# Performance work log

Measured on AMD Instinct MI355X. Metric: run time of the kernel, lower is better.

## Reference

```python
import jax, jax.numpy as jnp
import numpy as np

CHANNELS = 32


def _mlp(x, W1, b1, W2, b2, W3, b3):
    # FNN: Linear -> ReLU -> Linear -> ReLU -> Linear (last layer linear)
    h = jax.nn.relu(x @ W1 + b1)
    h = jax.nn.relu(h @ W2 + b2)
    return h @ W3 + b3


def setup_inputs() -> dict:
    key = jax.random.key(0)
    ks = jax.random.split(key, 8)
    E = 262144
    C = CHANNELS
    H = 128
    d_in = 4  # 2 * spatial_dim
    d_out = C * (C + 1)  # 1056
    s = lambda fan_in: 1.0 / np.sqrt(fan_in)
    return {
        "pos_i": jax.random.normal(ks[0], (E, 2), jnp.float32),
        "pos_j": jax.random.normal(ks[1], (E, 2), jnp.float32),
        "v_j": jax.random.normal(ks[2], (E, C), jnp.float32),
        "W1": jax.random.normal(ks[3], (d_in, H), jnp.float32) * s(d_in),
        "b1": jnp.zeros((H,), jnp.float32),
        "W2": jax.random.normal(ks[4], (H, H), jnp.float32) * s(H),
        "b2": jnp.zeros((H,), jnp.float32),
        "W3": jax.random.normal(ks[5], (H, d_out), jnp.float32) * s(H),
        "b3": jnp.zeros((d_out,), jnp.float32),
    }


def reference(pos_i, pos_j, v_j, W1, b1, W2, b2, W3, b3):
    C = CHANNELS
    pos_ij = jnp.concatenate((pos_i, pos_j), axis=-1)          # [E, 2*spatial_dim]
    kernel = _mlp(pos_ij, W1, b1, W2, b2, W3, b3)
    kernel = kernel.reshape(-1, C, C + 1)                      # [E, C, C+1]
    mat, bias = kernel[..., :, :-1], kernel[..., :, -1]        # [E,C,C], [E,C]
    return jnp.einsum('eij,ej->ei', mat, v_j) + bias           # [E, C]
```

## Files before the change

kernel.cpp:

```cpp
#include <hip/hip_runtime.h>


#define E_TOTAL 262144
#define EPB 256
#define NBLK (E_TOTAL / EPB)

typedef float f32x4 __attribute__((ext_vector_type(4)));
typedef short s8v  __attribute__((ext_vector_type(8)));

__device__ __forceinline__ unsigned short f2bf(float x) {
  unsigned u = __float_as_uint(x);
  u += 0x7fffu + ((u >> 16) & 1u);
  return (unsigned short)(u >> 16);
}

__global__ void prep_pack(const float* __restrict__ W2, const float* __restrict__ W3,
                          const float* __restrict__ b3,
                          unsigned short* __restrict__ Wg2, unsigned short* __restrict__ W2f,
                          unsigned short* __restrict__ b3f, float* __restrict__ b3c) {
  int idx = blockIdx.x * 256 + threadIdx.x;
  if (idx < 135168) {
    int jj = idx & 7, lane = (idx >> 3) & 63;
    int ksnn = idx >> 9, ks = ksnn & 3, nn = ksnn >> 2;
    int nnt = (nn < 33) ? (2 * nn) : (2 * (nn - 33) + 1);
    int k = ks * 32 + ((lane >> 4) << 3) + jj;
    int col = nnt * 16 + (lane & 15);
    int i = col & 31, j = col >> 5;
    Wg2[idx] = f2bf(W3[k * 1056 + i * 33 + j]);
  }
  if (idx < 16384) {
    int ks = idx >> 12, nt = (idx >> 9) & 7, l = (idx >> 3) & 63, jj = idx & 7;
    int k = ks * 32 + ((l >> 4) << 3) + jj;
    int n = nt * 16 + (l & 15);
    W2f[idx] = f2bf(W2[k * 128 + n]);
  }
  if (idx < 1024) {
    int jj = idx & 7, lane = (idx >> 3) & 63, ih = idx >> 9;
    int j = ((lane >> 4) << 3) + jj, i = ih * 16 + (lane & 15);
    b3f[idx] = f2bf(b3[i * 33 + j]);
  }
  if (idx < 32) b3c[idx] = b3[idx * 33 + 32];
}

template <int IH>
__device__ __forceinline__ void g_chunk(const unsigned short* __restrict__ buf,
                                        const float* __restrict__ vt,
                                        int j0, int lane, int eoff,
                                        const s8v (&af)[4][4], float (&oa)[2][4][4]) {
  const f32x4 zero4 = {0.f, 0.f, 0.f, 0.f};
#pragma unroll
  for (int t = 0; t < 3; ++t) {
    const int j = j0 + t;
    s8v bfr[4];
#pragma unroll
    for (int ks = 0; ks < 4; ++ks)
      bfr[ks] = *(const s8v*)&buf[(t * 4 + ks) * 512 + lane * 8];
    f32x4 p[4];
#pragma unroll
    for (int m = 0; m < 4; ++m) {
      p[m] = __builtin_amdgcn_mfma_f32_16x16x32_bf16(af[m][0], bfr[0], zero4, 0, 0, 0);
#pragma unroll
      for (int ks = 1; ks < 4; ++ks)
        p[m] = __builtin_amdgcn_mfma_f32_16x16x32_bf16(af[m][ks], bfr[ks], p[m], 0, 0, 0);
    }
    const float* vp = vt + j * 260 + eoff;
#pragma unroll
    for (int m = 0; m < 4; ++m) {
      f32x4 vv = *(const f32x4*)(vp + m * 16);
#pragma unroll
      for (int r = 0; r < 4; ++r) oa[IH][m][r] += vv[r] * p[m][r];
    }
  }
}

__global__ __launch_bounds__(256, 2) void fnn_fused(
    const float* __restrict__ pos_i, const float* __restrict__ pos_j,
    const float* __restrict__ vj, const float* __restrict__ W1,
    const float* __restrict__ b1, const float* __restrict__ b2,
    const unsigned short* __restrict__ W2f, const unsigned short* __restrict__ Wg2,
    const unsigned short* __restrict__ b3f, const float* __restrict__ b3c,
    float* __restrict__ out) {
  __shared__ __attribute__((aligned(16))) char smem[60432];
  float* vt = (float*)smem;
  unsigned short* h2n = (unsigned short*)(smem + 34320);
  unsigned short* h1c = (unsigned short*)(smem + 51728);
  unsigned short* Bb  = (unsigned short*)(smem + 34320);

  const int tid = threadIdx.x;
  const int w = tid >> 6, lane = tid & 63, q = lane >> 4, ln = lane & 15;
  const int B0 = blockIdx.x * EPB;
  const int eoff = w * 64 + q * 4;

  {
    const float* vrow = vj + (size_t)(B0 + tid) * 32;
#pragma unroll
    for (int j4 = 0; j4 < 8; ++j4) {
      float4 vv = *(const float4*)(vrow + j4 * 4);
      vt[(j4 * 4 + 0) * 260 + tid] = vv.x;
      vt[(j4 * 4 + 1) * 260 + tid] = vv.y;
      vt[(j4 * 4 + 2) * 260 + tid] = vv.z;
      vt[(j4 * 4 + 3) * 260 + tid] = vv.w;
    }
    vt[32 * 260 + tid] = 1.0f;
  }

  float oa[2][4][4];
  {
    s8v av[4];
#pragma unroll
    for (int m = 0; m < 4; ++m) {
      int e = B0 + w * 64 + m * 16 + ln;
      const float4 va = *(const float4*)(vj + (size_t)e * 32 + q * 8);
      const float4 vb = *(const float4*)(vj + (size_t)e * 32 + q * 8 + 4);
      s8v t;
      t[0] = (short)f2bf(va.x); t[1] = (short)f2bf(va.y);
      t[2] = (short)f2bf(va.z); t[3] = (short)f2bf(va.w);
      t[4] = (short)f2bf(vb.x); t[5] = (short)f2bf(vb.y);
      t[6] = (short)f2bf(vb.z); t[7] = (short)f2bf(vb.w);
      av[m] = t;
    }
#pragma unroll
    for (int ih = 0; ih < 2; ++ih) {
      s8v b3fr = *(const s8v*)(b3f + (ih * 64 + lane) * 8);
      float cbv = b3c[ih * 16 + ln];
      f32x4 ci = {cbv, cbv, cbv, cbv};
#pragma unroll
      for (int m = 0; m < 4; ++m) {
        f32x4 p = __builtin_amdgcn_mfma_f32_16x16x32_bf16(av[m], b3fr, ci, 0, 0, 0);
#pragma unroll
        for (int r = 0; r < 4; ++r) oa[ih][m][r] = p[r];
      }
    }
  }

  const int hh0 = (tid & 15) * 8;
  float w1r[4][8], b1r[8];
#pragma unroll
  for (int d = 0; d < 4; ++d)
#pragma unroll
    for (int u = 0; u < 8; ++u) w1r[d][u] = W1[d * 128 + hh0 + u];
#pragma unroll
  for (int u = 0; u < 8; ++u) b1r[u] = b1[hh0 + u];

  s8v af[4][4];
  for (int qtr = 0; qtr < 4; ++qtr) {
    for (int cb = 0; cb < 2; ++cb) {
#pragma unroll
      for (int half = 0; half < 2; ++half) {
        int ee = (tid >> 4) + half * 16;
        int eg = B0 + qtr * 64 + cb * 32 + ee;
        float2 pi = *(const float2*)(pos_i + (size_t)eg * 2);
        float2 pj = *(const float2*)(pos_j + (size_t)eg * 2);
        s8v hv;
#pragma unroll
        for (int u = 0; u < 8; ++u) {
          float o = b1r[u] + pi.x * w1r[0][u] + pi.y * w1r[1][u] +
                    pj.x * w1r[2][u] + pj.y * w1r[3][u];
          hv[u] = (short)f2bf(fmaxf(o, 0.f));
        }
        *(s8v*)&h1c[ee * 136 + hh0] = hv;
      }
      __syncthreads();
#pragma unroll
      for (int s = 0; s < 4; ++s) {
        int tt = w * 4 + s, mt = tt >> 3, nt = tt & 7;
        f32x4 a4 = {0.f, 0.f, 0.f, 0.f};
#pragma unroll
        for (int ks = 0; ks < 4; ++ks) {
          s8v afr = *(const s8v*)&h1c[(mt * 16 + ln) * 136 + ks * 32 + q * 8];
          s8v bfr = *(const s8v*)(W2f + ((ks * 8 + nt) * 64 + lane) * 8);
          a4 = __builtin_amdgcn_mfma_f32_16x16x32_bf16(afr, bfr, a4, 0, 0, 0);
        }
        float b2v = b2[nt * 16 + ln];
        int eb = cb * 32 + mt * 16 + q * 4;
        int kc = nt * 16 + ln;
#pragma unroll
        for (int r = 0; r < 4; ++r)
          h2n[(eb + r) * 136 + kc] = f2bf(fmaxf(a4[r] + b2v, 0.f));
      }
      __syncthreads();
    }
    if (w == qtr) {
#pragma unroll
      for (int m = 0; m < 4; ++m)
#pragma unroll
        for (int ks = 0; ks < 4; ++ks)
          af[m][ks] = *(const s8v*)&h2n[(m * 16 + ln) * 136 + ks * 32 + q * 8];
    }
    __syncthreads();
  }

  s8v pre[3];
#pragma unroll
  for (int t = 0; t < 3; ++t) pre[t] = *(const s8v*)(Wg2 + (t * 256 + tid) * 8);
#pragma unroll
  for (int t = 0; t < 3; ++t) *(s8v*)&Bb[(t * 256 + tid) * 8] = pre[t];
  __syncthreads();

  for (int c = 0; c < 22; ++c) {
    const int bb = c & 1;
    const unsigned short* buf = Bb + bb * 6144;
    if (c + 1 < 22) {
#pragma unroll
      for (int t = 0; t < 3; ++t)
        pre[t] = *(const s8v*)(Wg2 + (c + 1) * 6144 + (t * 256 + tid) * 8);
    }
    if (c < 11) g_chunk<0>(buf, vt, c * 3, lane, eoff, af, oa);
    else        g_chunk<1>(buf, vt, (c - 11) * 3, lane, eoff, af, oa);
    if (c + 1 < 22) {
      unsigned short* nb = Bb + (bb ^ 1) * 6144;
#pragma unroll
      for (int t = 0; t < 3; ++t) *(s8v*)&nb[(t * 256 + tid) * 8] = pre[t];
    }
    __syncthreads();
  }

#pragma unroll
  for (int m = 0; m < 4; ++m)
#pragma unroll
    for (int ih = 0; ih < 2; ++ih)
#pragma unroll
      for (int r = 0; r < 4; ++r) {
        int e = B0 + w * 64 + m * 16 + q * 4 + r;
        out[(size_t)e * 32 + ih * 16 + ln] = oa[ih][m][r];
      }
}

extern "C" void kernel_launch(void* const* d_in, const int* in_sizes, int n_in,
                              void* d_out, int out_size, void* d_ws, size_t ws_size,
                              hipStream_t stream) {
  const float* pos_i = (const float*)d_in[0];
  const float* pos_j = (const float*)d_in[1];
  const float* vj    = (const float*)d_in[2];
  const float* W1    = (const float*)d_in[3];
  const float* b1    = (const float*)d_in[4];
  const float* W2    = (const float*)d_in[5];
  const float* b2    = (const float*)d_in[6];
  const float* W3    = (const float*)d_in[7];
  const float* b3    = (const float*)d_in[8];
  float* outp = (float*)d_out;

  unsigned short* Wg2 = (unsigned short*)d_ws;
  unsigned short* W2f = (unsigned short*)((char*)d_ws + 270336);
  unsigned short* b3f = (unsigned short*)((char*)d_ws + 303104);
  float*          b3c = (float*)((char*)d_ws + 305152);

  prep_pack<<<528, 256, 0, stream>>>(W2, W3, b3, Wg2, W2f, b3f, b3c);
  fnn_fused<<<NBLK, 256, 0, stream>>>(pos_i, pos_j, vj, W1, b1, b2, W2f, Wg2, b3f, b3c, outp);
}
```

Measured before the change: 185.6 us.

## Stream W3 fragments from global into registers and drop LDS staging

Result: slower. 220.4 us (+18.8%).

```diff
diff --git a/kernel.cpp b/kernel.cpp
--- a/kernel.cpp
+++ b/kernel.cpp
@@ -43,34 +43,47 @@
 }
 
 template <int IH>
-__device__ __forceinline__ void g_chunk(const unsigned short* __restrict__ buf,
-                                        const float* __restrict__ vt,
-                                        int j0, int lane, int eoff,
-                                        const s8v (&af)[4][4], float (&oa)[2][4][4]) {
+__device__ __forceinline__ void g_tile(const s8v (&bfr)[4], const float* __restrict__ vt,
+                                       int j, int eoff,
+                                       const s8v (&af)[4][4], float (&oa)[2][4][4]) {
   const f32x4 zero4 = {0.f, 0.f, 0.f, 0.f};
-#pragma unroll
-  for (int t = 0; t < 3; ++t) {
-    const int j = j0 + t;
+  f32x4 p[4];
+#pragma unroll
+  for (int m = 0; m < 4; ++m)
+    p[m] = __builtin_amdgcn_mfma_f32_16x16x32_bf16(af[m][0], bfr[0], zero4, 0, 0, 0);
+#pragma unroll
+  for (int ks = 1; ks < 4; ++ks)
+#pragma unroll
+    for (int m = 0; m < 4; ++m)
+      p[m] = __builtin_amdgcn_mfma_f32_16x16x32_bf16(af[m][ks], bfr[ks], p[m], 0, 0, 0);
+  const float* vp = vt + j * 260 + eoff;
+#pragma unroll
+  for (int m = 0; m < 4; ++m) {
+    f32x4 vv = *(const f32x4*)(vp + m * 16);
+#pragma unroll
+    for (int r = 0; r < 4; ++r) oa[IH][m][r] += vv[r] * p[m][r];
+  }
+}
+
+template <int IH>
+__device__ __forceinline__ void g_pass(const unsigned short* __restrict__ Wg2,
+                                       const float* __restrict__ vt,
+                                       int lane, int eoff,
+                                       const s8v (&af)[4][4], float (&oa)[2][4][4]) {
+  const unsigned short* base = Wg2 + IH * 33 * 2048 + lane * 8;
+  s8v bnx[4];
+#pragma unroll
+  for (int ks = 0; ks < 4; ++ks) bnx[ks] = *(const s8v*)(base + ks * 512);
+  for (int j = 0; j < 32; ++j) {
     s8v bfr[4];
 #pragma unroll
+    for (int ks = 0; ks < 4; ++ks) bfr[ks] = bnx[ks];
+#pragma unroll
     for (int ks = 0; ks < 4; ++ks)
-      bfr[ks] = *(const s8v*)&buf[(t * 4 + ks) * 512 + lane * 8];
-    f32x4 p[4];
-#pragma unroll
-    for (int m = 0; m < 4; ++m) {
-      p[m] = __builtin_amdgcn_mfma_f32_16x16x32_bf16(af[m][0], bfr[0], zero4, 0, 0, 0);
-#pragma unroll
-      for (int ks = 1; ks < 4; ++ks)
-        p[m] = __builtin_amdgcn_mfma_f32_16x16x32_bf16(af[m][ks], bfr[ks], p[m], 0, 0, 0);
-    }
-    const float* vp = vt + j * 260 + eoff;
-#pragma unroll
-    for (int m = 0; m < 4; ++m) {
-      f32x4 vv = *(const f32x4*)(vp + m * 16);
-#pragma unroll
-      for (int r = 0; r < 4; ++r) oa[IH][m][r] += vv[r] * p[m][r];
-    }
-  }
+      bnx[ks] = *(const s8v*)(base + (j + 1) * 2048 + ks * 512);
+    g_tile<IH>(bfr, vt, j, eoff, af, oa);
+  }
+  g_tile<IH>(bnx, vt, 32, eoff, af, oa);
 }
 
 __global__ __launch_bounds__(256, 2) void fnn_fused(
@@ -80,29 +93,15 @@
     const unsigned short* __restrict__ W2f, const unsigned short* __restrict__ Wg2,
     const unsigned short* __restrict__ b3f, const float* __restrict__ b3c,
     float* __restrict__ out) {
-  __shared__ __attribute__((aligned(16))) char smem[60432];
+  __shared__ __attribute__((aligned(16))) char smem[36864];
   float* vt = (float*)smem;
-  unsigned short* h2n = (unsigned short*)(smem + 34320);
-  unsigned short* h1c = (unsigned short*)(smem + 51728);
-  unsigned short* Bb  = (unsigned short*)(smem + 34320);
+  unsigned short* h1c = (unsigned short*)smem;
+  unsigned short* h2n = (unsigned short*)(smem + 18432);
 
   const int tid = threadIdx.x;
   const int w = tid >> 6, lane = tid & 63, q = lane >> 4, ln = lane & 15;
   const int B0 = blockIdx.x * EPB;
   const int eoff = w * 64 + q * 4;
-
-  {
-    const float* vrow = vj + (size_t)(B0 + tid) * 32;
-#pragma unroll
-    for (int j4 = 0; j4 < 8; ++j4) {
-      float4 vv = *(const float4*)(vrow + j4 * 4);
-      vt[(j4 * 4 + 0) * 260 + tid] = vv.x;
-      vt[(j4 * 4 + 1) * 260 + tid] = vv.y;
-      vt[(j4 * 4 + 2) * 260 + tid] = vv.z;
-      vt[(j4 * 4 + 3) * 260 + tid] = vv.w;
-    }
-    vt[32 * 260 + tid] = 1.0f;
-  }
 
   float oa[2][4][4];
   {
@@ -134,86 +133,80 @@
   }
 
   const int hh0 = (tid & 15) * 8;
-  float w1r[4][8], b1r[8];
+  float w1r[4][8], b1r[8], b2r[8];
 #pragma unroll
   for (int d = 0; d < 4; ++d)
 #pragma unroll
     for (int u = 0; u < 8; ++u) w1r[d][u] = W1[d * 128 + hh0 + u];
 #pragma unroll
   for (int u = 0; u < 8; ++u) b1r[u] = b1[hh0 + u];
+#pragma unroll
+  for (int nt = 0; nt < 8; ++nt) b2r[nt] = b2[nt * 16 + ln];
 
   s8v af[4][4];
   for (int qtr = 0; qtr < 4; ++qtr) {
-    for (int cb = 0; cb < 2; ++cb) {
-#pragma unroll
-      for (int half = 0; half < 2; ++half) {
-        int ee = (tid >> 4) + half * 16;
-        int eg = B0 + qtr * 64 + cb * 32 + ee;
-        float2 pi = *(const float2*)(pos_i + (size_t)eg * 2);
-        float2 pj = *(const float2*)(pos_j + (size_t)eg * 2);
-        s8v hv;
-#pragma unroll
-        for (int u = 0; u < 8; ++u) {
-          float o = b1r[u] + pi.x * w1r[0][u] + pi.y * w1r[1][u] +
-                    pj.x * w1r[2][u] + pj.y * w1r[3][u];
-          hv[u] = (short)f2bf(fmaxf(o, 0.f));
+#pragma unroll
+    for (int half = 0; half < 4; ++half) {
+      int ee = (tid >> 4) + half * 16;
+      int eg = B0 + qtr * 64 + ee;
+      float2 pi = *(const float2*)(pos_i + (size_t)eg * 2);
+      float2 pj = *(const float2*)(pos_j + (size_t)eg * 2);
+      s8v hv;
+#pragma unroll
+      for (int u = 0; u < 8; ++u) {
+        float o = b1r[u] + pi.x * w1r[0][u] + pi.y * w1r[1][u] +
+                  pj.x * w1r[2][u] + pj.y * w1r[3][u];
+        hv[u] = (short)f2bf(fmaxf(o, 0.f));
+      }
+      *(s8v*)&h1c[ee * 144 + hh0] = hv;
+    }
+    __syncthreads();
+    {
+      s8v afr[4];
+#pragma unroll
+      for (int ks = 0; ks < 4; ++ks)
+        afr[ks] = *(const s8v*)&h1c[(w * 16 + ln) * 144 + ks * 32 + q * 8];
+#pragma unroll
+      for (int nt = 0; nt < 8; ++nt) {
+        f32x4 a4 = {0.f, 0.f, 0.f, 0.f};
+#pragma unroll
+        for (int ks = 0; ks < 4; ++ks) {
+          s8v bfr2 = *(const s8v*)(W2f + ((ks * 8 + nt) * 64 + lane) * 8);
+          a4 = __builtin_amdgcn_mfma_f32_16x16x32_bf16(afr[ks], bfr2, a4, 0, 0, 0);
         }
-        *(s8v*)&h1c[ee * 136 + hh0] = hv;
-      }
-      __syncthreads();
-#pragma unroll
-      for (int s = 0; s < 4; ++s) {
-        int tt = w * 4 + s, mt = tt >> 3, nt = tt & 7;
-        f32x4 a4 = {0.f, 0.f, 0.f, 0.f};
-#pragma unroll
-        for (int ks = 0; ks < 4; ++ks) {
-          s8v afr = *(const s8v*)&h1c[(mt * 16 + ln) * 136 + ks * 32 + q * 8];
-          s8v bfr = *(const s8v*)(W2f + ((ks * 8 + nt) * 64 + lane) * 8);
-          a4 = __builtin_amdgcn_mfma_f32_16x16x32_bf16(afr, bfr, a4, 0, 0, 0);
-        }
-        float b2v = b2[nt * 16 + ln];
-        int eb = cb * 32 + mt * 16 + q * 4;
-        int kc = nt * 16 + ln;
 #pragma unroll
         for (int r = 0; r < 4; ++r)
-          h2n[(eb + r) * 136 + kc] = f2bf(fmaxf(a4[r] + b2v, 0.f));
-      }
-      __syncthreads();
-    }
+          h2n[(w * 16 + q * 4 + r) * 144 + nt * 16 + ln] =
+              f2bf(fmaxf(a4[r] + b2r[nt], 0.f));
+      }
+    }
+    __syncthreads();
     if (w == qtr) {
 #pragma unroll
       for (int m = 0; m < 4; ++m)
 #pragma unroll
         for (int ks = 0; ks < 4; ++ks)
-          af[m][ks] = *(const s8v*)&h2n[(m * 16 + ln) * 136 + ks * 32 + q * 8];
-    }
-    __syncthreads();
-  }
-
-  s8v pre[3];
-#pragma unroll
-  for (int t = 0; t < 3; ++t) pre[t] = *(const s8v*)(Wg2 + (t * 256 + tid) * 8);
-#pragma unroll
-  for (int t = 0; t < 3; ++t) *(s8v*)&Bb[(t * 256 + tid) * 8] = pre[t];
+          af[m][ks] = *(const s8v*)&h2n[(m * 16 + ln) * 144 + ks * 32 + q * 8];
+    }
+  }
   __syncthreads();
 
-  for (int c = 0; c < 22; ++c) {
-    const int bb = c & 1;
-    const unsigned short* buf = Bb + bb * 6144;
-    if (c + 1 < 22) {
-#pragma unroll
-      for (int t = 0; t < 3; ++t)
-        pre[t] = *(const s8v*)(Wg2 + (c + 1) * 6144 + (t * 256 + tid) * 8);
-    }
-    if (c < 11) g_chunk<0>(buf, vt, c * 3, lane, eoff, af, oa);
-    else        g_chunk<1>(buf, vt, (c - 11) * 3, lane, eoff, af, oa);
-    if (c + 1 < 22) {
-      unsigned short* nb = Bb + (bb ^ 1) * 6144;
-#pragma unroll
-      for (int t = 0; t < 3; ++t) *(s8v*)&nb[(t * 256 + tid) * 8] = pre[t];
-    }
-    __syncthreads();
-  }
+  {
+    const float* vrow = vj + (size_t)(B0 + tid) * 32;
+#pragma unroll
+    for (int j4 = 0; j4 < 8; ++j4) {
+      float4 vv = *(const float4*)(vrow + j4 * 4);
+      vt[(j4 * 4 + 0) * 260 + tid] = vv.x;
+      vt[(j4 * 4 + 1) * 260 + tid] = vv.y;
+      vt[(j4 * 4 + 2) * 260 + tid] = vv.z;
+      vt[(j4 * 4 + 3) * 260 + tid] = vv.w;
+    }
+    vt[32 * 260 + tid] = 1.0f;
+  }
+  __syncthreads();
+
+  g_pass<0>(Wg2, vt, lane, eoff, af, oa);
+  g_pass<1>(Wg2, vt, lane, eoff, af, oa);
 
 #pragma unroll
   for (int m = 0; m < 4; ++m)
```
